# Performance work log

Hardware: AMD Instinct MI355X
Metric: run time of the kernel (lower is better)

## Reference

```python
import jax, jax.numpy as jnp
import numpy as np


def setup_inputs() -> dict:
    key = jax.random.key(0)
    kq, kk, kv = jax.random.split(key, 3)
    B, T, D = 8, 4096, 64
    q = jax.random.normal(kq, (B, T, D), dtype=jnp.float32)
    k = jax.random.normal(kk, (B, T, D), dtype=jnp.float32)
    v = jax.random.normal(kv, (B, T, D), dtype=jnp.float32)
    return {"q": q, "k": k, "v": v}


def reference(q, k, v):
    # q,k,v: [b, t, d]
    b, t_q, d = q.shape
    t_k = k.shape[1]
    scale = 1.0 / jnp.sqrt(jnp.asarray(d, dtype=q.dtype))
    qk = jnp.einsum('bqd,bkd->bqk', q, k) * scale  # [b, t_q, t_k]
    # causal mask: positions t2 > t1 set to -inf (replaces the Python double-loop)
    causal_mask = jnp.arange(t_k)[None, :] > jnp.arange(t_q)[:, None]  # [t_q, t_k]
    qk = jnp.where(causal_mask[None, :, :], -jnp.inf, qk)
    attn = jax.nn.softmax(qk, axis=-1)
    return jnp.einsum('bqk,bkd->bqd', attn, v)
```

## Files before the change

kernel.cpp:

```cpp
#include <hip/hip_runtime.h>

namespace {

constexpr float QSC = 0.18033688f;

typedef short bf16x8 __attribute__((ext_vector_type(8)));
typedef float f32x4 __attribute__((ext_vector_type(4)));

typedef __attribute__((address_space(3))) unsigned int lds_u32;
typedef __attribute__((address_space(1))) const unsigned int gbl_u32;

__device__ inline float exp2x(float x) { return __builtin_amdgcn_exp2f(x); }

__device__ inline unsigned int pack2(float a, float b) {
  unsigned int ua = __builtin_bit_cast(unsigned int, a);
  unsigned int ub = __builtin_bit_cast(unsigned int, b);
  ua = (ua + 0x8000u) >> 16;
  ub = (ub + 0x8000u) & 0xFFFF0000u;
  return ua | ub;
}

__device__ inline void gl_lds16(const unsigned short* g, unsigned short* l) {
  __builtin_amdgcn_global_load_lds((gbl_u32*)g, (lds_u32*)l, 16, 0, 0);
}

__device__ inline bf16x8 ld16(const unsigned short* p) {
  uint4 u = *(const uint4*)p;
  return __builtin_bit_cast(bf16x8, u);
}

__device__ inline void pswap32(unsigned int& a, unsigned int& b) {
  asm volatile("v_permlane32_swap_b32 %0, %1" : "+v"(a), "+v"(b));
}
__device__ inline void pswap16(unsigned int& a, unsigned int& b) {
  asm volatile("v_permlane16_swap_b32 %0, %1" : "+v"(a), "+v"(b));
}

__global__ __launch_bounds__(256) void prep(const float* __restrict__ K,
                                            const float* __restrict__ V,
                                            unsigned short* __restrict__ Kbf,
                                            unsigned short* __restrict__ Vtb) {
  __shared__ float Vl[64 * 65];
  const int bid = blockIdx.x;
  const int b = bid >> 6, kt = bid & 63;
  const int tid = threadIdx.x;
  const float4* Ks4 = (const float4*)(K + ((size_t)b * 4096 + kt * 64) * 64);
  const float4* Vs4 = (const float4*)(V + ((size_t)b * 4096 + kt * 64) * 64);
  #pragma unroll
  for (int i = 0; i < 4; ++i) {
    int idx = tid + 256 * i;
    int row = idx >> 4, c4 = idx & 15;
    float4 t = Ks4[idx];
    *(uint2*)&Kbf[((size_t)b * 4096 + kt * 64 + row) * 64 + c4 * 4] =
        make_uint2(pack2(t.x, t.y), pack2(t.z, t.w));
    float4 tv = Vs4[idx];
    float* d = &Vl[row * 65 + c4 * 4];
    d[0] = tv.x; d[1] = tv.y; d[2] = tv.z; d[3] = tv.w;
  }
  __syncthreads();
  #pragma unroll
  for (int i = 0; i < 4; ++i) {
    int idx = tid + 256 * i;
    int dd = idx >> 4, kc = idx & 15;
    float a  = Vl[(kc * 4 + 0) * 65 + dd];
    float b2 = Vl[(kc * 4 + 1) * 65 + dd];
    float c  = Vl[(kc * 4 + 2) * 65 + dd];
    float e  = Vl[(kc * 4 + 3) * 65 + dd];
    *(uint2*)&Vtb[((size_t)b * 64 + dd) * 4096 + kt * 64 + kc * 4] =
        make_uint2(pack2(a, b2), pack2(c, e));
  }
}

__launch_bounds__(512, 4)
__global__ void fa_mfma(const float* __restrict__ Q,
                        float* __restrict__ O,
                        const unsigned short* __restrict__ Kbf,
                        const unsigned short* __restrict__ Vtb) {
  __shared__ __align__(16) unsigned short smem[32768];

  const int bid = blockIdx.x;
  int b, qt;
  if (bid < 256) { b = bid & 7; qt = bid >> 3; }
  else           { b = bid & 7; qt = 63 - ((bid - 256) >> 3); }

  const int tid  = threadIdx.x;
  const int w    = tid >> 6;
  const int g    = w >> 2;
  const int wg   = w & 3;
  const int lane = tid & 63;
  const int quad = lane >> 4;
  const int lc   = lane & 15;

  unsigned short* Kb0 = &smem[(g * 2 + 0) * 4096];
  unsigned short* Kb1 = &smem[(g * 2 + 1) * 4096];
  unsigned short* Vb0 = &smem[16384 + (g * 2 + 0) * 4096];
  unsigned short* Vb1 = &smem[16384 + (g * 2 + 1) * 4096];

  const unsigned short* Kt_g = Kbf + (size_t)b * 4096 * 64;
  const unsigned short* Vt_g = Vtb + (size_t)b * 64 * 4096;

  const int r0 = wg * 16 + (lane >> 3);
  const int c0 = (lane & 7) ^ (r0 & 7);

  const int ph0 = (quad ^ (lc & 7)) * 8;
  const int ph1 = ((4 + quad) ^ (lc & 7)) * 8;

  const size_t base = (size_t)b * 4096 * 64;
  const float* Qb = Q + base + (size_t)qt * 64 * 64;
  float* Ob = O + base + (size_t)qt * 64 * 64;

  {
    const int kt0 = (g <= qt) ? g : qt;
    const unsigned short* gk = Kt_g + (size_t)(kt0 * 64) * 64;
    gl_lds16(gk + (size_t)r0 * 64 + c0 * 8, Kb0 + wg * 1024);
    gl_lds16(gk + (size_t)(r0 + 8) * 64 + c0 * 8, Kb0 + wg * 1024 + 512);
    const unsigned short* gv = Vt_g + kt0 * 64;
    gl_lds16(gv + (size_t)r0 * 4096 + c0 * 8, Vb0 + wg * 1024);
    gl_lds16(gv + (size_t)(r0 + 8) * 4096 + c0 * 8, Vb0 + wg * 1024 + 512);
  }

  bf16x8 qf[2];
  {
    const float* qrow = Qb + (wg * 16 + lc) * 64 + quad * 8;
    #pragma unroll
    for (int ks = 0; ks < 2; ++ks) {
      float4 x = *(const float4*)(qrow + ks * 32);
      float4 y = *(const float4*)(qrow + ks * 32 + 4);
      uint4 u = make_uint4(pack2(x.x * QSC, x.y * QSC), pack2(x.z * QSC, x.w * QSC),
                           pack2(y.x * QSC, y.y * QSC), pack2(y.z * QSC, y.w * QSC));
      qf[ks] = __builtin_bit_cast(bf16x8, u);
    }
  }

  float l_i = 0.0f;
  f32x4 o[4];
  #pragma unroll
  for (int nt = 0; nt < 4; ++nt) o[nt] = f32x4{0.f, 0.f, 0.f, 0.f};

  const int nIter = qt / 2 + 1;
  for (int i = 0; i < nIter; ++i) {
    const int kt = 2 * i + g;
    const bool active = (kt <= qt);
    unsigned short* Kcur = (i & 1) ? Kb1 : Kb0;
    unsigned short* Vcur = (i & 1) ? Vb1 : Vb0;
    unsigned short* Knxt = (i & 1) ? Kb0 : Kb1;
    unsigned short* Vnxt = (i & 1) ? Vb0 : Vb1;

    asm volatile("s_waitcnt vmcnt(0)" ::: "memory");
    __builtin_amdgcn_s_barrier();

    {
      int ktn = 2 * (i + 1) + g; if (ktn > qt) ktn = qt;
      const unsigned short* gk = Kt_g + (size_t)(ktn * 64) * 64;
      gl_lds16(gk + (size_t)r0 * 64 + c0 * 8, Knxt + wg * 1024);
      gl_lds16(gk + (size_t)(r0 + 8) * 64 + c0 * 8, Knxt + wg * 1024 + 512);
      const unsigned short* gv = Vt_g + ktn * 64;
      gl_lds16(gv + (size_t)r0 * 4096 + c0 * 8, Vnxt + wg * 1024);
      gl_lds16(gv + (size_t)(r0 + 8) * 4096 + c0 * 8, Vnxt + wg * 1024 + 512);
    }

    if (active) {
      f32x4 st[4];
      __builtin_amdgcn_s_setprio(1);
      #pragma unroll
      for (int t = 0; t < 4; ++t) {
        f32x4 c = {0.f, 0.f, 0.f, 0.f};
        c = __builtin_amdgcn_mfma_f32_16x16x32_bf16(ld16(&Kcur[(t * 16 + lc) * 64 + ph0]), qf[0], c, 0, 0, 0);
        c = __builtin_amdgcn_mfma_f32_16x16x32_bf16(ld16(&Kcur[(t * 16 + lc) * 64 + ph1]), qf[1], c, 0, 0, 0);
        st[t] = c;
      }
      __builtin_amdgcn_s_setprio(0);

      const bool diag = (kt == qt);
      const int qrow = wg * 16 + lc;
      unsigned int pc[4][2];
      #pragma unroll
      for (int t = 0; t < 4; ++t) {
        float e[4];
        #pragma unroll
        for (int r = 0; r < 4; ++r) {
          int key_l = 16 * t + quad * 4 + r;
          float v = st[t][r];
          if (diag && key_l > qrow) v = -1e30f;
          e[r] = exp2x(v);
        }
        l_i += (e[0] + e[1]) + (e[2] + e[3]);
        pc[t][0] = pack2(e[0], e[1]);
        pc[t][1] = pack2(e[2], e[3]);
      }

      __builtin_amdgcn_s_setprio(1);
      #pragma unroll
      for (int ks = 0; ks < 2; ++ks) {
        unsigned int x0 = pc[2 * ks][0], y0 = pc[2 * ks + 1][0];
        unsigned int x1 = pc[2 * ks][1], y1 = pc[2 * ks + 1][1];
        pswap32(x0, y0); pswap16(x0, y0);
        pswap32(x1, y1); pswap16(x1, y1);
        bf16x8 a = __builtin_bit_cast(bf16x8, make_uint4(x0, x1, y0, y1));
        const int ph = ks ? ph1 : ph0;
        #pragma unroll
        for (int nt = 0; nt < 4; ++nt) {
          o[nt] = __builtin_amdgcn_mfma_f32_16x16x32_bf16(a, ld16(&Vcur[(nt * 16 + lc) * 64 + ph]), o[nt], 0, 0, 0);
        }
      }
      __builtin_amdgcn_s_setprio(0);
    }
  }

  __syncthreads();

  l_i += __shfl_xor(l_i, 16);
  l_i += __shfl_xor(l_i, 32);

  constexpr int MSTR = 66;
  float* mrg = (float*)smem;
  if (g == 1) {
    #pragma unroll
    for (int r = 0; r < 4; ++r) {
      int row = wg * 16 + quad * 4 + r;
      #pragma unroll
      for (int nt = 0; nt < 4; ++nt)
        mrg[row * MSTR + nt * 16 + lc] = o[nt][r];
    }
    if (quad == 0)
      mrg[64 * MSTR + wg * 16 + lc] = l_i;
  }
  __syncthreads();
  if (g == 0) {
    const int row0 = wg * 16 + lc;
    float linv = 1.0f / (l_i + mrg[64 * MSTR + row0]);
    float lv[4];
    #pragma unroll
    for (int r = 0; r < 4; ++r) lv[r] = __shfl(linv, quad * 4 + r);
    #pragma unroll
    for (int r = 0; r < 4; ++r) {
      int row = wg * 16 + quad * 4 + r;
      float* orow = Ob + row * 64 + lc;
      #pragma unroll
      for (int nt = 0; nt < 4; ++nt) {
        float o1 = mrg[row * MSTR + nt * 16 + lc];
        orow[nt * 16] = (o[nt][r] + o1) * lv[r];
      }
    }
  }
}

}

extern "C" void kernel_launch(void* const* d_in, const int* in_sizes, int n_in,
                              void* d_out, int out_size, void* d_ws, size_t ws_size,
                              hipStream_t stream) {
  const float* q = (const float*)d_in[0];
  const float* k = (const float*)d_in[1];
  const float* v = (const float*)d_in[2];
  float* out = (float*)d_out;
  unsigned short* Kbf = (unsigned short*)d_ws;
  unsigned short* Vtb = Kbf + (size_t)8 * 4096 * 64;
  prep<<<dim3(512), dim3(256), 0, stream>>>(k, v, Kbf, Vtb);
  fa_mfma<<<dim3(512), dim3(512), 0, stream>>>(q, out, Kbf, Vtb);
}
```

Baseline: 120.4 us.

## Drop intra-block key split; use single 4-wave group per query tile

Replaces the two-group key-tile split inside each 512-thread block with a single 256-thread group that walks all key tiles sequentially. The final LDS merge of partial outputs and row sums goes away, as does the per-iteration active-flag branch. The diagonal tile is peeled out so only the last iteration applies the causal mask. Blocks now run longest query tiles first, use half the LDS and allow more resident blocks, but each block's serial chain of key tiles becomes twice as long.

Result: slower. 135.5 us (+12.6%).

```diff
diff --git a/kernel.cpp b/kernel.cpp
--- a/kernel.cpp
+++ b/kernel.cpp
@@ -71,30 +71,27 @@
   }
 }
 
-__launch_bounds__(512, 4)
+__launch_bounds__(256, 5)
 __global__ void fa_mfma(const float* __restrict__ Q,
                         float* __restrict__ O,
                         const unsigned short* __restrict__ Kbf,
                         const unsigned short* __restrict__ Vtb) {
-  __shared__ __align__(16) unsigned short smem[32768];
+  __shared__ __align__(16) unsigned short smem[16384];
 
   const int bid = blockIdx.x;
-  int b, qt;
-  if (bid < 256) { b = bid & 7; qt = bid >> 3; }
-  else           { b = bid & 7; qt = 63 - ((bid - 256) >> 3); }
+  const int b  = bid & 7;
+  const int qt = 63 - (bid >> 3);
 
   const int tid  = threadIdx.x;
-  const int w    = tid >> 6;
-  const int g    = w >> 2;
-  const int wg   = w & 3;
+  const int wg   = tid >> 6;
   const int lane = tid & 63;
   const int quad = lane >> 4;
   const int lc   = lane & 15;
 
-  unsigned short* Kb0 = &smem[(g * 2 + 0) * 4096];
-  unsigned short* Kb1 = &smem[(g * 2 + 1) * 4096];
-  unsigned short* Vb0 = &smem[16384 + (g * 2 + 0) * 4096];
-  unsigned short* Vb1 = &smem[16384 + (g * 2 + 1) * 4096];
+  unsigned short* Kb0 = smem;
+  unsigned short* Kb1 = smem + 4096;
+  unsigned short* Vb0 = smem + 8192;
+  unsigned short* Vb1 = smem + 12288;
 
   const unsigned short* Kt_g = Kbf + (size_t)b * 4096 * 64;
   const unsigned short* Vt_g = Vtb + (size_t)b * 64 * 4096;
@@ -109,15 +106,10 @@
   const float* Qb = Q + base + (size_t)qt * 64 * 64;
   float* Ob = O + base + (size_t)qt * 64 * 64;
 
-  {
-    const int kt0 = (g <= qt) ? g : qt;
-    const unsigned short* gk = Kt_g + (size_t)(kt0 * 64) * 64;
-    gl_lds16(gk + (size_t)r0 * 64 + c0 * 8, Kb0 + wg * 1024);
-    gl_lds16(gk + (size_t)(r0 + 8) * 64 + c0 * 8, Kb0 + wg * 1024 + 512);
-    const unsigned short* gv = Vt_g + kt0 * 64;
-    gl_lds16(gv + (size_t)r0 * 4096 + c0 * 8, Vb0 + wg * 1024);
-    gl_lds16(gv + (size_t)(r0 + 8) * 4096 + c0 * 8, Vb0 + wg * 1024 + 512);
-  }
+  gl_lds16(Kt_g + (size_t)r0 * 64 + c0 * 8, Kb0 + wg * 1024);
+  gl_lds16(Kt_g + (size_t)(r0 + 8) * 64 + c0 * 8, Kb0 + wg * 1024 + 512);
+  gl_lds16(Vt_g + (size_t)r0 * 4096 + c0 * 8, Vb0 + wg * 1024);
+  gl_lds16(Vt_g + (size_t)(r0 + 8) * 4096 + c0 * 8, Vb0 + wg * 1024 + 512);
 
   bf16x8 qf[2];
   {
@@ -137,110 +129,96 @@
   #pragma unroll
   for (int nt = 0; nt < 4; ++nt) o[nt] = f32x4{0.f, 0.f, 0.f, 0.f};
 
-  const int nIter = qt / 2 + 1;
-  for (int i = 0; i < nIter; ++i) {
-    const int kt = 2 * i + g;
-    const bool active = (kt <= qt);
-    unsigned short* Kcur = (i & 1) ? Kb1 : Kb0;
-    unsigned short* Vcur = (i & 1) ? Vb1 : Vb0;
+  const int qrow = wg * 16 + lc;
+
+  auto body = [&](const unsigned short* Kcur, const unsigned short* Vcur, bool diag) __attribute__((always_inline)) {
+    f32x4 st[4];
+    __builtin_amdgcn_s_setprio(1);
+    #pragma unroll
+    for (int t = 0; t < 4; ++t) {
+      f32x4 c = {0.f, 0.f, 0.f, 0.f};
+      c = __builtin_amdgcn_mfma_f32_16x16x32_bf16(ld16(&Kcur[(t * 16 + lc) * 64 + ph0]), qf[0], c, 0, 0, 0);
+      c = __builtin_amdgcn_mfma_f32_16x16x32_bf16(ld16(&Kcur[(t * 16 + lc) * 64 + ph1]), qf[1], c, 0, 0, 0);
+      st[t] = c;
+    }
+    __builtin_amdgcn_s_setprio(0);
+
+    unsigned int pc[4][2];
+    #pragma unroll
+    for (int t = 0; t < 4; ++t) {
+      float e[4];
+      #pragma unroll
+      for (int r = 0; r < 4; ++r) {
+        float v = st[t][r];
+        if (diag) {
+          int key_l = 16 * t + quad * 4 + r;
+          if (key_l > qrow) v = -1e30f;
+        }
+        e[r] = exp2x(v);
+      }
+      l_i += (e[0] + e[1]) + (e[2] + e[3]);
+      pc[t][0] = pack2(e[0], e[1]);
+      pc[t][1] = pack2(e[2], e[3]);
+    }
+
+    __builtin_amdgcn_s_setprio(1);
+    #pragma unroll
+    for (int ks = 0; ks < 2; ++ks) {
+      unsigned int x0 = pc[2 * ks][0], y0 = pc[2 * ks + 1][0];
+      unsigned int x1 = pc[2 * ks][1], y1 = pc[2 * ks + 1][1];
+      pswap32(x0, y0); pswap16(x0, y0);
+      pswap32(x1, y1); pswap16(x1, y1);
+      bf16x8 a = __builtin_bit_cast(bf16x8, make_uint4(x0, x1, y0, y1));
+      const int ph = ks ? ph1 : ph0;
+      #pragma unroll
+      for (int nt = 0; nt < 4; ++nt) {
+        o[nt] = __builtin_amdgcn_mfma_f32_16x16x32_bf16(a, ld16(&Vcur[(nt * 16 + lc) * 64 + ph]), o[nt], 0, 0, 0);
+      }
+    }
+    __builtin_amdgcn_s_setprio(0);
+  };
+
+  for (int i = 0; i < qt; ++i) {
+    const unsigned short* Kcur = (i & 1) ? Kb1 : Kb0;
+    const unsigned short* Vcur = (i & 1) ? Vb1 : Vb0;
     unsigned short* Knxt = (i & 1) ? Kb0 : Kb1;
     unsigned short* Vnxt = (i & 1) ? Vb0 : Vb1;
 
     asm volatile("s_waitcnt vmcnt(0)" ::: "memory");
     __builtin_amdgcn_s_barrier();
 
-    {
-      int ktn = 2 * (i + 1) + g; if (ktn > qt) ktn = qt;
-      const unsigned short* gk = Kt_g + (size_t)(ktn * 64) * 64;
-      gl_lds16(gk + (size_t)r0 * 64 + c0 * 8, Knxt + wg * 1024);
-      gl_lds16(gk + (size_t)(r0 + 8) * 64 + c0 * 8, Knxt + wg * 1024 + 512);
-      const unsigned short* gv = Vt_g + ktn * 64;
-      gl_lds16(gv + (size_t)r0 * 4096 + c0 * 8, Vnxt + wg * 1024);
-      gl_lds16(gv + (size_t)(r0 + 8) * 4096 + c0 * 8, Vnxt + wg * 1024 + 512);
-    }
-
-    if (active) {
-      f32x4 st[4];
-      __builtin_amdgcn_s_setprio(1);
-      #pragma unroll
-      for (int t = 0; t < 4; ++t) {
-        f32x4 c = {0.f, 0.f, 0.f, 0.f};
-        c = __builtin_amdgcn_mfma_f32_16x16x32_bf16(ld16(&Kcur[(t * 16 + lc) * 64 + ph0]), qf[0], c, 0, 0, 0);
-        c = __builtin_amdgcn_mfma_f32_16x16x32_bf16(ld16(&Kcur[(t * 16 + lc) * 64 + ph1]), qf[1], c, 0, 0, 0);
-        st[t] = c;
-      }
-      __builtin_amdgcn_s_setprio(0);
-
-      const bool diag = (kt == qt);
-      const int qrow = wg * 16 + lc;
-      unsigned int pc[4][2];
-      #pragma unroll
-      for (int t = 0; t < 4; ++t) {
-        float e[4];
-        #pragma unroll
-        for (int r = 0; r < 4; ++r) {
-          int key_l = 16 * t + quad * 4 + r;
-          float v = st[t][r];
-          if (diag && key_l > qrow) v = -1e30f;
-          e[r] = exp2x(v);
-        }
-        l_i += (e[0] + e[1]) + (e[2] + e[3]);
-        pc[t][0] = pack2(e[0], e[1]);
-        pc[t][1] = pack2(e[2], e[3]);
-      }
-
-      __builtin_amdgcn_s_setprio(1);
-      #pragma unroll
-      for (int ks = 0; ks < 2; ++ks) {
-        unsigned int x0 = pc[2 * ks][0], y0 = pc[2 * ks + 1][0];
-        unsigned int x1 = pc[2 * ks][1], y1 = pc[2 * ks + 1][1];
-        pswap32(x0, y0); pswap16(x0, y0);
-        pswap32(x1, y1); pswap16(x1, y1);
-        bf16x8 a = __builtin_bit_cast(bf16x8, make_uint4(x0, x1, y0, y1));
-        const int ph = ks ? ph1 : ph0;
-        #pragma unroll
-        for (int nt = 0; nt < 4; ++nt) {
-          o[nt] = __builtin_amdgcn_mfma_f32_16x16x32_bf16(a, ld16(&Vcur[(nt * 16 + lc) * 64 + ph]), o[nt], 0, 0, 0);
-        }
-      }
-      __builtin_amdgcn_s_setprio(0);
-    }
-  }
-
-  __syncthreads();
+    const unsigned short* gk = Kt_g + (size_t)((i + 1) * 64) * 64;
+    gl_lds16(gk + (size_t)r0 * 64 + c0 * 8, Knxt + wg * 1024);
+    gl_lds16(gk + (size_t)(r0 + 8) * 64 + c0 * 8, Knxt + wg * 1024 + 512);
+    const unsigned short* gv = Vt_g + (i + 1) * 64;
+    gl_lds16(gv + (size_t)r0 * 4096 + c0 * 8, Vnxt + wg * 1024);
+    gl_lds16(gv + (size_t)(r0 + 8) * 4096 + c0 * 8, Vnxt + wg * 1024 + 512);
+
+    body(Kcur, Vcur, false);
+  }
+
+  {
+    const unsigned short* Kcur = (qt & 1) ? Kb1 : Kb0;
+    const unsigned short* Vcur = (qt & 1) ? Vb1 : Vb0;
+    asm volatile("s_waitcnt vmcnt(0)" ::: "memory");
+    __builtin_amdgcn_s_barrier();
+    body(Kcur, Vcur, true);
+  }
 
   l_i += __shfl_xor(l_i, 16);
   l_i += __shfl_xor(l_i, 32);
-
-  constexpr int MSTR = 66;
-  float* mrg = (float*)smem;
-  if (g == 1) {
-    #pragma unroll
-    for (int r = 0; r < 4; ++r) {
-      int row = wg * 16 + quad * 4 + r;
-      #pragma unroll
-      for (int nt = 0; nt < 4; ++nt)
-        mrg[row * MSTR + nt * 16 + lc] = o[nt][r];
-    }
-    if (quad == 0)
-      mrg[64 * MSTR + wg * 16 + lc] = l_i;
-  }
-  __syncthreads();
-  if (g == 0) {
-    const int row0 = wg * 16 + lc;
-    float linv = 1.0f / (l_i + mrg[64 * MSTR + row0]);
-    float lv[4];
-    #pragma unroll
-    for (int r = 0; r < 4; ++r) lv[r] = __shfl(linv, quad * 4 + r);
-    #pragma unroll
-    for (int r = 0; r < 4; ++r) {
-      int row = wg * 16 + quad * 4 + r;
-      float* orow = Ob + row * 64 + lc;
-      #pragma unroll
-      for (int nt = 0; nt < 4; ++nt) {
-        float o1 = mrg[row * MSTR + nt * 16 + lc];
-        orow[nt * 16] = (o[nt][r] + o1) * lv[r];
-      }
+  float linv = 1.0f / l_i;
+  float lv[4];
+  #pragma unroll
+  for (int r = 0; r < 4; ++r) lv[r] = __shfl(linv, quad * 4 + r);
+
+  #pragma unroll
+  for (int r = 0; r < 4; ++r) {
+    int row = wg * 16 + quad * 4 + r;
+    float* orow = Ob + row * 64 + lc;
+    #pragma unroll
+    for (int nt = 0; nt < 4; ++nt) {
+      orow[nt * 16] = o[nt][r] * lv[r];
     }
   }
 }
@@ -257,5 +235,5 @@
   unsigned short* Kbf = (unsigned short*)d_ws;
   unsigned short* Vtb = Kbf + (size_t)8 * 4096 * 64;
   prep<<<dim3(512), dim3(256), 0, stream>>>(k, v, Kbf, Vtb);
-  fa_mfma<<<dim3(512), dim3(512), 0, stream>>>(q, out, Kbf, Vtb);
-}
+  fa_mfma<<<dim3(512), dim3(256), 0, stream>>>(q, out, Kbf, Vtb);
+}
```
